# Performance work log

Hardware: AMD Instinct MI355X
Metric: run time of the kernel (lower is better)

The kernel has to match this reference:

```python
import jax, jax.numpy as jnp
import numpy as np

N, D_FEAT, T, H = 4000, 6, 60, 64


def _gru_layer(inp, Wih, Whh, bih, bhh):
    # inp: [N, T, in]; torch GRU gate math, gate order (r, z, n)
    x_proj = inp @ Wih.T + bih  # [N, T, 3H]
    h0 = jnp.zeros((inp.shape[0], Whh.shape[1]), inp.dtype)

    def step(h, xp):
        gh = h @ Whh.T + bhh
        xr, xz, xn = jnp.split(xp, 3, axis=-1)
        hr, hz, hn = jnp.split(gh, 3, axis=-1)
        r = jax.nn.sigmoid(xr + hr)
        z = jax.nn.sigmoid(xz + hz)
        n = jnp.tanh(xn + r * hn)
        h = (1.0 - z) * n + z * h
        return h, h

    _, hs = jax.lax.scan(step, h0, jnp.transpose(x_proj, (1, 0, 2)))  # [T, N, H]
    return jnp.transpose(hs, (1, 0, 2))  # [N, T, H]


def setup_inputs():
    key = jax.random.key(0)
    ks = jax.random.split(key, 16)
    s = 1.0 / np.sqrt(H)
    u = lambda k, shape: jax.random.uniform(k, shape, jnp.float32, -s, s)
    inp = {
        "x": jax.random.normal(ks[0], (N, D_FEAT * T), jnp.float32),
        "relation_matrix": jax.random.randint(ks[1], (N, N, 3), 0, 2).astype(jnp.float32),
        "W_ih0": u(ks[2], (3 * H, D_FEAT)),
        "W_hh0": u(ks[3], (3 * H, H)),
        "b_ih0": u(ks[4], (3 * H,)),
        "b_hh0": u(ks[5], (3 * H,)),
        "W_ih1": u(ks[6], (3 * H, H)),
        "W_hh1": u(ks[7], (3 * H, H)),
        "b_ih1": u(ks[8], (3 * H,)),
        "b_hh1": u(ks[9], (3 * H,)),
        "W": jax.random.normal(ks[10], (2 * H, 1), jnp.float32) * np.sqrt(6.0 / (2 * H + 1)),
        "b": jnp.zeros((), jnp.float32),
        "fc_w": u(ks[11], (1, 2 * H)),
        "fc_b": u(ks[12], (1,)),
    }
    return inp


def reference(x, relation_matrix, W_ih0, W_hh0, b_ih0, b_hh0,
              W_ih1, W_hh1, b_ih1, b_hh1, W, b, fc_w, fc_b):
    n = x.shape[0]
    # [N, d_feat*T] -> [N, T, d_feat]
    xh = jnp.transpose(x.reshape(n, D_FEAT, -1), (0, 2, 1))
    xh = _gru_layer(xh, W_ih0, W_hh0, b_ih0, b_hh0)
    xh = _gru_layer(xh, W_ih1, W_hh1, b_ih1, b_hh1)
    x_hidden = xh[:, -1, :]  # [N, H]

    # concat(ei, hidden_batch) @ W == a_i + c_j  (avoid O(N^2 * 2H) tensor)
    a = x_hidden @ W[:H, 0]   # [N]
    c = x_hidden @ W[H:, 0]   # [N]
    weight = jax.nn.leaky_relu(a[:, None] + c[None, :] + b, 0.01)  # [N, N]

    mask = relation_matrix.sum(axis=2)  # [N, N]
    valid_weight = jnp.where(mask == 0, -1000000.0, mask * weight)
    valid_weight = jax.nn.softmax(valid_weight, axis=1)

    hidden = valid_weight @ x_hidden            # [N, H]
    hidden = jnp.concatenate([x_hidden, hidden], axis=1)  # [N, 2H]
    pred = (hidden @ fc_w.T + fc_b).squeeze()   # [N]
    return pred
```

## Files before the change

kernel.cpp:

```cpp
#include <hip/hip_runtime.h>

#define NR 4000
#define TS 60
#define DF 6
#define HD 64
#define MB 16
#define ARB 32

typedef __attribute__((ext_vector_type(8))) short bf8_t;
typedef __attribute__((ext_vector_type(4))) short bf4_t;
typedef __attribute__((ext_vector_type(4))) float f32x4;

__device__ __forceinline__ float sigf(float x) { return 1.0f / (1.0f + __expf(-x)); }
__device__ __forceinline__ float tanhfast(float x) { return 1.0f - 2.0f / (1.0f + __expf(2.0f * x)); }

__device__ __forceinline__ unsigned short f2bf(float v) {
  union { float f; unsigned u; } x; x.f = v;
  unsigned r = (x.u + 0x7fffu + ((x.u >> 16) & 1u)) >> 16;
  return (unsigned short)r;
}
__device__ __forceinline__ float bf2f(unsigned short h) {
  union { unsigned u; float f; } y; y.u = ((unsigned)h) << 16; return y.f;
}
__device__ __forceinline__ void split8(const float* v, bf8_t& hi, bf8_t& lo) {
#pragma unroll
  for (int j = 0; j < 8; ++j) {
    unsigned short h = f2bf(v[j]);
    float rem = v[j] - bf2f(h);
    hi[j] = (short)h;
    lo[j] = (short)f2bf(rem);
  }
}

__global__ __launch_bounds__(256, 1) void gru_mfma(
    const float* __restrict__ x,
    const float* __restrict__ Wih0, const float* __restrict__ Whh0,
    const float* __restrict__ bih0, const float* __restrict__ bhh0,
    const float* __restrict__ Wih1, const float* __restrict__ Whh1,
    const float* __restrict__ bih1, const float* __restrict__ bhh1,
    const float* __restrict__ Wac,
    float* __restrict__ xh_out, float* __restrict__ a_out, float* __restrict__ c_out) {
  __shared__ float xldsT[TS][MB][12];
  __shared__ __align__(16) unsigned short h0hiL[2][16][76];
  __shared__ __align__(16) unsigned short h0loL[2][16][76];
  __shared__ __align__(16) unsigned short h1hiL[2][16][76];
  __shared__ __align__(16) unsigned short h1loL[2][16][76];
  __shared__ float red[2][4][MB];

  const int tid = threadIdx.x;
  const int w = tid >> 6;
  const int lane = tid & 63;
  const int lg = lane >> 4;
  const int lm = lane & 15;
  const int unit = w * 16 + lm;
  const int r0 = blockIdx.x * MB;

  for (int idx = tid; idx < MB * 360; idx += 256) {
    int rr = idx / 360, cc = idx - rr * 360;
    int f = cc / 60, t = cc - f * 60;
    xldsT[t][rr][f] = x[(size_t)r0 * 360 + idx];
  }

  bf8_t wB[3][3][2][2];
  {
    const float* mats[3] = {Whh0, Wih1, Whh1};
#pragma unroll
    for (int m = 0; m < 3; ++m)
#pragma unroll
      for (int g = 0; g < 3; ++g)
#pragma unroll
        for (int kt = 0; kt < 2; ++kt) {
          const float* src = mats[m] + (size_t)(g * 64 + unit) * 64 + kt * 32 + 8 * lg;
          float v[8];
          *(float4*)&v[0] = *(const float4*)&src[0];
          *(float4*)&v[4] = *(const float4*)&src[4];
          split8(v, wB[m][g][kt][0], wB[m][g][kt][1]);
        }
  }
  float wih0g[3][DF];
#pragma unroll
  for (int g = 0; g < 3; ++g)
#pragma unroll
    for (int f = 0; f < DF; ++f)
      wih0g[g][f] = Wih0[(size_t)(g * 64 + unit) * DF + f];

  const float bi0r = bih0[unit], bi0z = bih0[64 + unit], bi0n = bih0[128 + unit];
  const float bh0r = bhh0[unit], bh0z = bhh0[64 + unit], bh0n = bhh0[128 + unit];
  const float c1R = bih1[unit] + bhh1[unit];
  const float c1Z = bih1[64 + unit] + bhh1[64 + unit];
  const float b1xn = bih1[128 + unit], b1hn = bhh1[128 + unit];

  bf8_t a0[2][2], a1[2][2];
  bf8_t zf = {};
#pragma unroll
  for (int kt = 0; kt < 2; ++kt)
#pragma unroll
    for (int h = 0; h < 2; ++h) { a0[kt][h] = zf; a1[kt][h] = zf; }
  float h0c[4] = {0.f, 0.f, 0.f, 0.f};
  float h1c[4] = {0.f, 0.f, 0.f, 0.f};

  __syncthreads();

#define MF(acc, A, B) acc = __builtin_amdgcn_mfma_f32_16x16x32_bf16(A, B, acc, 0, 0, 0)
#define MF3(acc, Af, Bf) do { \
    MF(acc, Af[0], Bf[0]); MF(acc, Af[0], Bf[1]); MF(acc, Af[1], Bf[0]); } while (0)

  for (int p = 0; p <= TS; ++p) {
    const bool doL0 = (p < TS);
    const bool doL1 = (p >= 1);
    const int par = p & 1;
    f32x4 aR, aZ, aN;
    float xn0[4];
    if (doL0) {
#pragma unroll
      for (int i = 0; i < 4; ++i) {
        const int row = 4 * lg + i;
        const float* xb = &xldsT[p][row][0];
        float4 x4 = *(const float4*)xb;
        float2 x2 = *(const float2*)(xb + 4);
        float sr = bi0r, sz = bi0z, sn = bi0n;
        sr = fmaf(wih0g[0][0], x4.x, sr); sz = fmaf(wih0g[1][0], x4.x, sz); sn = fmaf(wih0g[2][0], x4.x, sn);
        sr = fmaf(wih0g[0][1], x4.y, sr); sz = fmaf(wih0g[1][1], x4.y, sz); sn = fmaf(wih0g[2][1], x4.y, sn);
        sr = fmaf(wih0g[0][2], x4.z, sr); sz = fmaf(wih0g[1][2], x4.z, sz); sn = fmaf(wih0g[2][2], x4.z, sn);
        sr = fmaf(wih0g[0][3], x4.w, sr); sz = fmaf(wih0g[1][3], x4.w, sz); sn = fmaf(wih0g[2][3], x4.w, sn);
        sr = fmaf(wih0g[0][4], x2.x, sr); sz = fmaf(wih0g[1][4], x2.x, sz); sn = fmaf(wih0g[2][4], x2.x, sn);
        sr = fmaf(wih0g[0][5], x2.y, sr); sz = fmaf(wih0g[1][5], x2.y, sz); sn = fmaf(wih0g[2][5], x2.y, sn);
        aR[i] = sr + bh0r;
        aZ[i] = sz + bh0z;
        aN[i] = bh0n;
        xn0[i] = sn;
      }
#pragma unroll
      for (int kt = 0; kt < 2; ++kt) {
        MF3(aR, a0[kt], wB[0][0][kt]);
        MF3(aZ, a0[kt], wB[0][1][kt]);
        MF3(aN, a0[kt], wB[0][2][kt]);
      }
    }
    f32x4 R1, Z1, XN, HN;
    if (doL1) {
#pragma unroll
      for (int i = 0; i < 4; ++i) { R1[i] = c1R; Z1[i] = c1Z; XN[i] = b1xn; HN[i] = b1hn; }
#pragma unroll
      for (int kt = 0; kt < 2; ++kt) {
        MF3(R1, a0[kt], wB[1][0][kt]);
        MF3(Z1, a0[kt], wB[1][1][kt]);
        MF3(XN, a0[kt], wB[1][2][kt]);
        MF3(R1, a1[kt], wB[2][0][kt]);
        MF3(Z1, a1[kt], wB[2][1][kt]);
        MF3(HN, a1[kt], wB[2][2][kt]);
      }
    }
    if (doL0) {
#pragma unroll
      for (int i = 0; i < 4; ++i) {
        float r = sigf(aR[i]);
        float z = sigf(aZ[i]);
        float n = tanhfast(xn0[i] + r * aN[i]);
        h0c[i] = n + z * (h0c[i] - n);
        const int row = 4 * lg + i;
        unsigned u = __float_as_uint(h0c[i]);
        h0hiL[par][row][unit] = (unsigned short)(u >> 16);
        float lo = h0c[i] - __uint_as_float(u & 0xffff0000u);
        h0loL[par][row][unit] = (unsigned short)(__float_as_uint(lo) >> 16);
      }
    }
    if (doL1) {
#pragma unroll
      for (int i = 0; i < 4; ++i) {
        float r = sigf(R1[i]);
        float z = sigf(Z1[i]);
        float n = tanhfast(XN[i] + r * HN[i]);
        h1c[i] = n + z * (h1c[i] - n);
      }
      if (p < TS) {
#pragma unroll
        for (int i = 0; i < 4; ++i) {
          const int row = 4 * lg + i;
          unsigned u = __float_as_uint(h1c[i]);
          h1hiL[par][row][unit] = (unsigned short)(u >> 16);
          float lo = h1c[i] - __uint_as_float(u & 0xffff0000u);
          h1loL[par][row][unit] = (unsigned short)(__float_as_uint(lo) >> 16);
        }
      }
    }
    __syncthreads();
    if (p < TS) {
#pragma unroll
      for (int kt = 0; kt < 2; ++kt) {
        const int cb = kt * 32 + 8 * lg;
        bf4_t u0 = *(const bf4_t*)&h0hiL[par][lm][cb];
        bf4_t u1 = *(const bf4_t*)&h0hiL[par][lm][cb + 4];
        a0[kt][0] = __builtin_shufflevector(u0, u1, 0, 1, 2, 3, 4, 5, 6, 7);
        bf4_t l0 = *(const bf4_t*)&h0loL[par][lm][cb];
        bf4_t l1 = *(const bf4_t*)&h0loL[par][lm][cb + 4];
        a0[kt][1] = __builtin_shufflevector(l0, l1, 0, 1, 2, 3, 4, 5, 6, 7);
      }
      if (p >= 1) {
#pragma unroll
        for (int kt = 0; kt < 2; ++kt) {
          const int cb = kt * 32 + 8 * lg;
          bf4_t u0 = *(const bf4_t*)&h1hiL[par][lm][cb];
          bf4_t u1 = *(const bf4_t*)&h1hiL[par][lm][cb + 4];
          a1[kt][0] = __builtin_shufflevector(u0, u1, 0, 1, 2, 3, 4, 5, 6, 7);
          bf4_t l0 = *(const bf4_t*)&h1loL[par][lm][cb];
          bf4_t l1 = *(const bf4_t*)&h1loL[par][lm][cb + 4];
          a1[kt][1] = __builtin_shufflevector(l0, l1, 0, 1, 2, 3, 4, 5, 6, 7);
        }
      }
    }
  }
#undef MF3
#undef MF

#pragma unroll
  for (int i = 0; i < 4; ++i)
    xh_out[(size_t)(r0 + 4 * lg + i) * HD + unit] = h1c[i];

  const float WaU = Wac[unit], WcU = Wac[64 + unit];
#pragma unroll
  for (int i = 0; i < 4; ++i) {
    float av = h1c[i] * WaU, cv = h1c[i] * WcU;
#pragma unroll
    for (int off = 1; off < 16; off <<= 1) {
      av += __shfl_xor(av, off, 64);
      cv += __shfl_xor(cv, off, 64);
    }
    if (lm == 0) {
      red[0][w][4 * lg + i] = av;
      red[1][w][4 * lg + i] = cv;
    }
  }
  __syncthreads();
  if (tid < MB) {
    a_out[r0 + tid] = red[0][0][tid] + red[0][1][tid] + red[0][2][tid] + red[0][3][tid];
    c_out[r0 + tid] = red[1][0][tid] + red[1][1][tid] + red[1][2][tid] + red[1][3][tid];
  }
}

__global__ __launch_bounds__(256) void attn_part(
    const float* __restrict__ rel,
    const float* __restrict__ xh,
    const float* __restrict__ aArr, const float* __restrict__ cArr,
    const float* __restrict__ bSc,
    float* __restrict__ part, int jsl, int lsp) {
  __shared__ float xhl[64][68];
  __shared__ float pbuf[ARB][64];
  __shared__ float cls[1024];

  const int tid = threadIdx.x;
  const int rg = tid >> 5;
  const int tk = tid & 31;
  const int bx = blockIdx.x;
  const int ib = bx >> lsp;
  const int js = bx & ((1 << lsp) - 1);
  const int jbeg = js * jsl;
  const int jend = (jbeg + jsl < NR) ? (jbeg + jsl) : NR;
  const int nch = (jend - jbeg + 63) >> 6;
  const float bb = bSc[0];

  int irow[4];
  float aib[4];
#pragma unroll
  for (int rr = 0; rr < 4; ++rr) {
    irow[rr] = ib * ARB + rg + 8 * rr;
    aib[rr] = aArr[irow[rr]] + bb;
  }

  for (int t = tid; t < jsl; t += 256)
    cls[t] = (jbeg + t < NR) ? cArr[jbeg + t] : 0.f;

  float pr[4][6];
#pragma unroll
  for (int rr = 0; rr < 4; ++rr) {
    const float* rp = rel + (size_t)irow[rr] * (3 * NR) + (size_t)(jbeg + 2 * tk) * 3;
#pragma unroll
    for (int e = 0; e < 6; ++e) pr[rr][e] = rp[e];
  }

  float m[4], s[4], acc0[4], acc1[4];
#pragma unroll
  for (int rr = 0; rr < 4; ++rr) { m[rr] = -3.0e38f; s[rr] = 0.f; acc0[rr] = 0.f; acc1[rr] = 0.f; }

  for (int c = 0; c < nch; ++c) {
    const int j0 = jbeg + c * 64;
    __syncthreads();
    {
      const int jj = tid >> 2, seg = tid & 3;
      const int j = j0 + jj;
      if (j < NR) {
        const float4* src = (const float4*)(xh + (size_t)j * 64 + seg * 16);
#pragma unroll
        for (int q = 0; q < 4; ++q) *(float4*)&xhl[jj][seg * 16 + 4 * q] = src[q];
      } else {
        float4 z = {0.f, 0.f, 0.f, 0.f};
#pragma unroll
        for (int q = 0; q < 4; ++q) *(float4*)&xhl[jj][seg * 16 + 4 * q] = z;
      }
    }

    const int jb = j0 + 2 * tk;
    const bool ok = (jb < jend);
    const int ci = c * 64 + 2 * tk;
    const float cl0 = cls[ci], cl1 = cls[ci + 1];

#pragma unroll
    for (int rr = 0; rr < 4; ++rr) {
      float msum0 = pr[rr][0] + pr[rr][1] + pr[rr][2];
      float msum1 = pr[rr][3] + pr[rr][4] + pr[rr][5];
      float w0 = aib[rr] + cl0, w1 = aib[rr] + cl1;
      w0 = (w0 > 0.f) ? w0 : 0.01f * w0;
      w1 = (w1 > 0.f) ? w1 : 0.01f * w1;
      float v0 = (!ok) ? -3.0e37f : ((msum0 == 0.f) ? -1.0e6f : msum0 * w0);
      float v1 = (!ok) ? -3.0e37f : ((msum1 == 0.f) ? -1.0e6f : msum1 * w1);

      float lm2 = fmaxf(v0, v1);
#pragma unroll
      for (int off = 16; off; off >>= 1) lm2 = fmaxf(lm2, __shfl_xor(lm2, off, 32));
      const float mn = fmaxf(m[rr], lm2);
      const float f = __expf(m[rr] - mn);
      const float p0 = __expf(v0 - mn);
      const float p1 = __expf(v1 - mn);
      float ls = p0 + p1;
#pragma unroll
      for (int off = 16; off; off >>= 1) ls += __shfl_xor(ls, off, 32);
      s[rr] = s[rr] * f + ls;
      acc0[rr] *= f;
      acc1[rr] *= f;
      m[rr] = mn;
      pbuf[rg + 8 * rr][2 * tk] = p0;
      pbuf[rg + 8 * rr][2 * tk + 1] = p1;
    }

    if (c + 1 < nch) {
      const int jn = j0 + 64 + 2 * tk;
      if (jn < jend) {
#pragma unroll
        for (int rr = 0; rr < 4; ++rr) {
          const float* rp = rel + (size_t)irow[rr] * (3 * NR) + (size_t)jn * 3;
#pragma unroll
          for (int e = 0; e < 6; ++e) pr[rr][e] = rp[e];
        }
      }
    }

    __syncthreads();

#pragma unroll 2
    for (int j4 = 0; j4 < 16; ++j4) {
      float4 pv0 = *(const float4*)&pbuf[rg][4 * j4];
      float4 pv1 = *(const float4*)&pbuf[rg + 8][4 * j4];
      float4 pv2 = *(const float4*)&pbuf[rg + 16][4 * j4];
      float4 pv3 = *(const float4*)&pbuf[rg + 24][4 * j4];
      float2 x0 = *(const float2*)&xhl[4 * j4 + 0][2 * tk];
      float2 x1 = *(const float2*)&xhl[4 * j4 + 1][2 * tk];
      float2 x2 = *(const float2*)&xhl[4 * j4 + 2][2 * tk];
      float2 x3 = *(const float2*)&xhl[4 * j4 + 3][2 * tk];
      acc0[0] = fmaf(pv0.x, x0.x, acc0[0]); acc1[0] = fmaf(pv0.x, x0.y, acc1[0]);
      acc0[0] = fmaf(pv0.y, x1.x, acc0[0]); acc1[0] = fmaf(pv0.y, x1.y, acc1[0]);
      acc0[0] = fmaf(pv0.z, x2.x, acc0[0]); acc1[0] = fmaf(pv0.z, x2.y, acc1[0]);
      acc0[0] = fmaf(pv0.w, x3.x, acc0[0]); acc1[0] = fmaf(pv0.w, x3.y, acc1[0]);
      acc0[1] = fmaf(pv1.x, x0.x, acc0[1]); acc1[1] = fmaf(pv1.x, x0.y, acc1[1]);
      acc0[1] = fmaf(pv1.y, x1.x, acc0[1]); acc1[1] = fmaf(pv1.y, x1.y, acc1[1]);
      acc0[1] = fmaf(pv1.z, x2.x, acc0[1]); acc1[1] = fmaf(pv1.z, x2.y, acc1[1]);
      acc0[1] = fmaf(pv1.w, x3.x, acc0[1]); acc1[1] = fmaf(pv1.w, x3.y, acc1[1]);
      acc0[2] = fmaf(pv2.x, x0.x, acc0[2]); acc1[2] = fmaf(pv2.x, x0.y, acc1[2]);
      acc0[2] = fmaf(pv2.y, x1.x, acc0[2]); acc1[2] = fmaf(pv2.y, x1.y, acc1[2]);
      acc0[2] = fmaf(pv2.z, x2.x, acc0[2]); acc1[2] = fmaf(pv2.z, x2.y, acc1[2]);
      acc0[2] = fmaf(pv2.w, x3.x, acc0[2]); acc1[2] = fmaf(pv2.w, x3.y, acc1[2]);
      acc0[3] = fmaf(pv3.x, x0.x, acc0[3]); acc1[3] = fmaf(pv3.x, x0.y, acc1[3]);
      acc0[3] = fmaf(pv3.y, x1.x, acc0[3]); acc1[3] = fmaf(pv3.y, x1.y, acc1[3]);
      acc0[3] = fmaf(pv3.z, x2.x, acc0[3]); acc1[3] = fmaf(pv3.z, x2.y, acc1[3]);
      acc0[3] = fmaf(pv3.w, x3.x, acc0[3]); acc1[3] = fmaf(pv3.w, x3.y, acc1[3]);
    }
  }

#pragma unroll
  for (int rr = 0; rr < 4; ++rr) {
    float* base = part + ((size_t)bx * ARB + rg + 8 * rr) * 66;
    if (tk == 0) { base[0] = m[rr]; base[1] = s[rr]; }
    base[2 + 2 * tk] = acc0[rr];
    base[3 + 2 * tk] = acc1[rr];
  }
}

__global__ __launch_bounds__(256) void attn_combine(
    const float* __restrict__ part,
    const float* __restrict__ xh,
    const float* __restrict__ fcw, const float* __restrict__ fcb,
    float* __restrict__ pred, int nsplit) {
  const int tid = threadIdx.x;
  const int r = blockIdx.x * 4 + (tid >> 6);
  const int lane = tid & 63;
  const int ib = r / ARB, il = r % ARB;

  float mstar = -3.0e38f;
  for (int k = 0; k < nsplit; ++k) {
    const float* b = part + ((size_t)(ib * nsplit + k) * ARB + il) * 66;
    mstar = fmaxf(mstar, b[0]);
  }
  float sstar = 0.f, onum = 0.f;
  for (int k = 0; k < nsplit; ++k) {
    const float* b = part + ((size_t)(ib * nsplit + k) * ARB + il) * 66;
    const float wk = __expf(b[0] - mstar);
    sstar = fmaf(wk, b[1], sstar);
    onum = fmaf(wk, b[2 + lane], onum);
  }
  const float o = onum / sstar;
  float p = fcw[lane] * xh[(size_t)r * HD + lane] + fcw[64 + lane] * o;
#pragma unroll
  for (int off = 32; off; off >>= 1) p += __shfl_xor(p, off, 64);
  if (lane == 0) pred[r] = p + fcb[0];
}

extern "C" void kernel_launch(void* const* d_in, const int* in_sizes, int n_in,
                              void* d_out, int out_size, void* d_ws, size_t ws_size,
                              hipStream_t stream) {
  const float* x    = (const float*)d_in[0];
  const float* rel  = (const float*)d_in[1];
  const float* Wih0 = (const float*)d_in[2];
  const float* Whh0 = (const float*)d_in[3];
  const float* bih0 = (const float*)d_in[4];
  const float* bhh0 = (const float*)d_in[5];
  const float* Wih1 = (const float*)d_in[6];
  const float* Whh1 = (const float*)d_in[7];
  const float* bih1 = (const float*)d_in[8];
  const float* bhh1 = (const float*)d_in[9];
  const float* Wac  = (const float*)d_in[10];
  const float* bSc  = (const float*)d_in[11];
  const float* fcw  = (const float*)d_in[12];
  const float* fcb  = (const float*)d_in[13];

  float* xh   = (float*)d_ws;
  float* aA   = xh + (size_t)NR * HD;
  float* cA   = aA + NR;
  float* part = cA + NR;
  float* pred = (float*)d_out;

  const size_t headF = (size_t)NR * HD + 2 * NR;
  int nsplit = 16, lsp = 4;
  for (;;) {
    size_t needB = (headF + (size_t)(NR / ARB) * nsplit * ARB * 66) * 4;
    if (needB <= ws_size || nsplit == 4) break;
    nsplit >>= 1;
    lsp -= 1;
  }
  const int jsl = NR / nsplit;

  gru_mfma<<<NR / MB, 256, 0, stream>>>(x, Wih0, Whh0, bih0, bhh0, Wih1, Whh1,
                                        bih1, bhh1, Wac, xh, aA, cA);
  attn_part<<<(NR / ARB) * nsplit, 256, 0, stream>>>(rel, xh, aA, cA, bSc, part, jsl, lsp);
  attn_combine<<<NR / 4, 256, 0, stream>>>(part, xh, fcw, fcb, pred, nsplit);
}
```

Before: 184.6 us.

## Precompute uint8 relation mask sums in spare blocks alongside GRU kernel

Adds extra blocks to the GRU launch that stream the 192MB relation tensor and write a per-pair uint8 mask sum. This overlaps the dominant memory read with the latency-bound recurrent GRU work, which only uses a few blocks per CU. The attention kernel then reads 1 byte per pair instead of 12 bytes. The default split count also drops from 16 to 8, and an extra 16MB workspace write and read are added, with a fallback path when the workspace is too small.

```diff
diff --git a/kernel.cpp b/kernel.cpp
--- a/kernel.cpp
+++ b/kernel.cpp
@@ -6,6 +6,8 @@
 #define HD 64
 #define MB 16
 #define ARB 32
+#define GRUB (NR / MB)
+#define MSB 750
 
 typedef __attribute__((ext_vector_type(8))) short bf8_t;
 typedef __attribute__((ext_vector_type(4))) short bf4_t;
@@ -32,14 +34,16 @@
   }
 }
 
-__global__ __launch_bounds__(256, 1) void gru_mfma(
+__global__ __launch_bounds__(256, 1) void gru_and_msum(
     const float* __restrict__ x,
+    const float* __restrict__ rel,
     const float* __restrict__ Wih0, const float* __restrict__ Whh0,
     const float* __restrict__ bih0, const float* __restrict__ bhh0,
     const float* __restrict__ Wih1, const float* __restrict__ Whh1,
     const float* __restrict__ bih1, const float* __restrict__ bhh1,
     const float* __restrict__ Wac,
-    float* __restrict__ xh_out, float* __restrict__ a_out, float* __restrict__ c_out) {
+    float* __restrict__ xh_out, float* __restrict__ a_out, float* __restrict__ c_out,
+    unsigned char* __restrict__ msum8) {
   __shared__ float xldsT[TS][MB][12];
   __shared__ __align__(16) unsigned short h0hiL[2][16][76];
   __shared__ __align__(16) unsigned short h0loL[2][16][76];
@@ -48,12 +52,31 @@
   __shared__ float red[2][4][MB];
 
   const int tid = threadIdx.x;
+  const int bx = blockIdx.x;
+
+  if (bx >= GRUB) {
+    const int nmb = gridDim.x - GRUB;
+    const size_t ngroups = (size_t)NR * NR / 4;
+    const size_t stride = (size_t)nmb * 256;
+    for (size_t g = (size_t)(bx - GRUB) * 256 + tid; g < ngroups; g += stride) {
+      const float4* rp = (const float4*)(rel + 12 * g);
+      float4 v0 = rp[0], v1 = rp[1], v2 = rp[2];
+      uchar4 o;
+      o.x = (unsigned char)(v0.x + v0.y + v0.z);
+      o.y = (unsigned char)(v0.w + v1.x + v1.y);
+      o.z = (unsigned char)(v1.z + v1.w + v2.x);
+      o.w = (unsigned char)(v2.y + v2.z + v2.w);
+      *(uchar4*)&msum8[4 * g] = o;
+    }
+    return;
+  }
+
   const int w = tid >> 6;
   const int lane = tid & 63;
   const int lg = lane >> 4;
   const int lm = lane & 15;
   const int unit = w * 16 + lm;
-  const int r0 = blockIdx.x * MB;
+  const int r0 = bx * MB;
 
   for (int idx = tid; idx < MB * 360; idx += 256) {
     int rr = idx / 360, cc = idx - rr * 360;
@@ -238,15 +261,17 @@
   }
 }
 
+template <int UM>
 __global__ __launch_bounds__(256) void attn_part(
     const float* __restrict__ rel,
+    const unsigned char* __restrict__ msum8,
     const float* __restrict__ xh,
     const float* __restrict__ aArr, const float* __restrict__ cArr,
     const float* __restrict__ bSc,
     float* __restrict__ part, int jsl, int lsp) {
   __shared__ float xhl[64][68];
   __shared__ float pbuf[ARB][64];
-  __shared__ float cls[1024];
+  __shared__ float cls[2048];
 
   const int tid = threadIdx.x;
   const int rg = tid >> 5;
@@ -271,11 +296,16 @@
     cls[t] = (jbeg + t < NR) ? cArr[jbeg + t] : 0.f;
 
   float pr[4][6];
+  uchar2 pm[4];
 #pragma unroll
   for (int rr = 0; rr < 4; ++rr) {
-    const float* rp = rel + (size_t)irow[rr] * (3 * NR) + (size_t)(jbeg + 2 * tk) * 3;
-#pragma unroll
-    for (int e = 0; e < 6; ++e) pr[rr][e] = rp[e];
+    if (UM) {
+      pm[rr] = *(const uchar2*)&msum8[(size_t)irow[rr] * NR + jbeg + 2 * tk];
+    } else {
+      const float* rp = rel + (size_t)irow[rr] * (3 * NR) + (size_t)(jbeg + 2 * tk) * 3;
+#pragma unroll
+      for (int e = 0; e < 6; ++e) pr[rr][e] = rp[e];
+    }
   }
 
   float m[4], s[4], acc0[4], acc1[4];
@@ -306,8 +336,14 @@
 
 #pragma unroll
     for (int rr = 0; rr < 4; ++rr) {
-      float msum0 = pr[rr][0] + pr[rr][1] + pr[rr][2];
-      float msum1 = pr[rr][3] + pr[rr][4] + pr[rr][5];
+      float msum0, msum1;
+      if (UM) {
+        msum0 = (float)pm[rr].x;
+        msum1 = (float)pm[rr].y;
+      } else {
+        msum0 = pr[rr][0] + pr[rr][1] + pr[rr][2];
+        msum1 = pr[rr][3] + pr[rr][4] + pr[rr][5];
+      }
       float w0 = aib[rr] + cl0, w1 = aib[rr] + cl1;
       w0 = (w0 > 0.f) ? w0 : 0.01f * w0;
       w1 = (w1 > 0.f) ? w1 : 0.01f * w1;
@@ -337,9 +373,13 @@
       if (jn < jend) {
 #pragma unroll
         for (int rr = 0; rr < 4; ++rr) {
-          const float* rp = rel + (size_t)irow[rr] * (3 * NR) + (size_t)jn * 3;
-#pragma unroll
-          for (int e = 0; e < 6; ++e) pr[rr][e] = rp[e];
+          if (UM) {
+            pm[rr] = *(const uchar2*)&msum8[(size_t)irow[rr] * NR + jn];
+          } else {
+            const float* rp = rel + (size_t)irow[rr] * (3 * NR) + (size_t)jn * 3;
+#pragma unroll
+            for (int e = 0; e < 6; ++e) pr[rr][e] = rp[e];
+          }
         }
       }
     }
@@ -431,24 +471,42 @@
   const float* fcw  = (const float*)d_in[12];
   const float* fcb  = (const float*)d_in[13];
 
-  float* xh   = (float*)d_ws;
-  float* aA   = xh + (size_t)NR * HD;
-  float* cA   = aA + NR;
+  float* xh = (float*)d_ws;
+  float* aA = xh + (size_t)NR * HD;
+  float* cA = aA + NR;
   float* part = cA + NR;
   float* pred = (float*)d_out;
 
   const size_t headF = (size_t)NR * HD + 2 * NR;
-  int nsplit = 16, lsp = 4;
-  for (;;) {
-    size_t needB = (headF + (size_t)(NR / ARB) * nsplit * ARB * 66) * 4;
-    if (needB <= ws_size || nsplit == 4) break;
-    nsplit >>= 1;
-    lsp -= 1;
+  const size_t msumB = (size_t)NR * NR;
+  auto needB = [&](int ns, bool um) {
+    return (headF + (size_t)(NR / ARB) * ns * ARB * 66) * 4 + (um ? msumB : 0);
+  };
+  bool use_msum = true;
+  int nsplit = 8, lsp = 3;
+  if (needB(8, true) > ws_size) {
+    if (needB(4, true) <= ws_size) { nsplit = 4; lsp = 2; }
+    else if (needB(2, true) <= ws_size) { nsplit = 2; lsp = 1; }
+    else {
+      use_msum = false;
+      if (needB(8, false) <= ws_size) { nsplit = 8; lsp = 3; }
+      else { nsplit = 4; lsp = 2; }
+    }
   }
   const int jsl = NR / nsplit;
-
-  gru_mfma<<<NR / MB, 256, 0, stream>>>(x, Wih0, Whh0, bih0, bhh0, Wih1, Whh1,
-                                        bih1, bhh1, Wac, xh, aA, cA);
-  attn_part<<<(NR / ARB) * nsplit, 256, 0, stream>>>(rel, xh, aA, cA, bSc, part, jsl, lsp);
+  unsigned char* msum8 =
+      (unsigned char*)(part + (size_t)(NR / ARB) * nsplit * ARB * 66);
+
+  const int nblk = use_msum ? (GRUB + MSB) : GRUB;
+  gru_and_msum<<<nblk, 256, 0, stream>>>(x, rel, Wih0, Whh0, bih0, bhh0,
+                                         Wih1, Whh1, bih1, bhh1, Wac,
+                                         xh, aA, cA, msum8);
+  if (use_msum) {
+    attn_part<1><<<(NR / ARB) * nsplit, 256, 0, stream>>>(
+        rel, msum8, xh, aA, cA, bSc, part, jsl, lsp);
+  } else {
+    attn_part<0><<<(NR / ARB) * nsplit, 256, 0, stream>>>(
+        rel, msum8, xh, aA, cA, bSc, part, jsl, lsp);
+  }
   attn_combine<<<NR / 4, 256, 0, stream>>>(part, xh, fcw, fcb, pred, nsplit);
 }
```

Result: slower. 207.8 us (+12.6%).

## Stage relation-matrix tiles through LDS with coalesced float4 loads, fix split at 8

Applied to the files above, without the earlier changes.

Adds a specialised attention-partial kernel that loads each 64-column chunk of the 32 relation rows into shared memory with wide float4 loads. Before this, each thread loaded six scalars per row into registers. The kernel is specialised to 8 column splits with constant trip counts, down from the previous default of 16. It targets the cost of streaming the large relation tensor with narrow per-thread loads. In exchange it drops the register prefetch of the next chunk and adds an extra barrier per chunk. Its larger shared-memory footprint may also lower occupancy. The old path is kept as a fallback when the workspace is small.

```diff
diff --git a/kernel.cpp b/kernel.cpp
--- a/kernel.cpp
+++ b/kernel.cpp
@@ -238,25 +238,26 @@
   }
 }
 
-__global__ __launch_bounds__(256) void attn_part(
+__global__ __launch_bounds__(256) void attn_part_lds(
     const float* __restrict__ rel,
     const float* __restrict__ xh,
     const float* __restrict__ aArr, const float* __restrict__ cArr,
     const float* __restrict__ bSc,
-    float* __restrict__ part, int jsl, int lsp) {
+    float* __restrict__ part) {
   __shared__ float xhl[64][68];
   __shared__ float pbuf[ARB][64];
-  __shared__ float cls[1024];
+  __shared__ float cls[512];
+  __shared__ float relL[32][200];
 
   const int tid = threadIdx.x;
   const int rg = tid >> 5;
   const int tk = tid & 31;
   const int bx = blockIdx.x;
-  const int ib = bx >> lsp;
-  const int js = bx & ((1 << lsp) - 1);
+  const int ib = bx >> 3;
+  const int js = bx & 7;
+  const int jsl = NR / 8;
   const int jbeg = js * jsl;
-  const int jend = (jbeg + jsl < NR) ? (jbeg + jsl) : NR;
-  const int nch = (jend - jbeg + 63) >> 6;
+  const int jend = jbeg + jsl;
   const float bb = bSc[0];
 
   int irow[4];
@@ -267,22 +268,14 @@
     aib[rr] = aArr[irow[rr]] + bb;
   }
 
-  for (int t = tid; t < jsl; t += 256)
-    cls[t] = (jbeg + t < NR) ? cArr[jbeg + t] : 0.f;
-
-  float pr[4][6];
-#pragma unroll
-  for (int rr = 0; rr < 4; ++rr) {
-    const float* rp = rel + (size_t)irow[rr] * (3 * NR) + (size_t)(jbeg + 2 * tk) * 3;
-#pragma unroll
-    for (int e = 0; e < 6; ++e) pr[rr][e] = rp[e];
-  }
+  for (int t = tid; t < 512; t += 256)
+    cls[t] = (t < jsl) ? cArr[jbeg + t] : 0.f;
 
   float m[4], s[4], acc0[4], acc1[4];
 #pragma unroll
   for (int rr = 0; rr < 4; ++rr) { m[rr] = -3.0e38f; s[rr] = 0.f; acc0[rr] = 0.f; acc1[rr] = 0.f; }
 
-  for (int c = 0; c < nch; ++c) {
+  for (int c = 0; c < 8; ++c) {
     const int j0 = jbeg + c * 64;
     __syncthreads();
     {
@@ -298,6 +291,17 @@
         for (int q = 0; q < 4; ++q) *(float4*)&xhl[jj][seg * 16 + 4 * q] = z;
       }
     }
+#pragma unroll
+    for (int k = 0; k < 6; ++k) {
+      const int fidx = k * 256 + tid;
+      const int sg = fidx / 48;
+      const int q = fidx - sg * 48;
+      int fo = j0 * 3 + 4 * q;
+      if (fo > 12000 - 4) fo = 0;
+      const float4 v = *(const float4*)(rel + (size_t)(ib * 32 + sg) * 12000 + fo);
+      *(float4*)&relL[sg][4 * q] = v;
+    }
+    __syncthreads();
 
     const int jb = j0 + 2 * tk;
     const bool ok = (jb < jend);
@@ -306,8 +310,12 @@
 
 #pragma unroll
     for (int rr = 0; rr < 4; ++rr) {
-      float msum0 = pr[rr][0] + pr[rr][1] + pr[rr][2];
-      float msum1 = pr[rr][3] + pr[rr][4] + pr[rr][5];
+      const int qp = rg + 8 * rr;
+      float2 f0 = *(const float2*)&relL[qp][6 * tk];
+      float2 f1 = *(const float2*)&relL[qp][6 * tk + 2];
+      float2 f2 = *(const float2*)&relL[qp][6 * tk + 4];
+      float msum0 = f0.x + f0.y + f1.x;
+      float msum1 = f1.y + f2.x + f2.y;
       float w0 = aib[rr] + cl0, w1 = aib[rr] + cl1;
       w0 = (w0 > 0.f) ? w0 : 0.01f * w0;
       w1 = (w1 > 0.f) ? w1 : 0.01f * w1;
@@ -331,20 +339,6 @@
       pbuf[rg + 8 * rr][2 * tk] = p0;
       pbuf[rg + 8 * rr][2 * tk + 1] = p1;
     }
-
-    if (c + 1 < nch) {
-      const int jn = j0 + 64 + 2 * tk;
-      if (jn < jend) {
-#pragma unroll
-        for (int rr = 0; rr < 4; ++rr) {
-          const float* rp = rel + (size_t)irow[rr] * (3 * NR) + (size_t)jn * 3;
-#pragma unroll
-          for (int e = 0; e < 6; ++e) pr[rr][e] = rp[e];
-        }
-      }
-    }
-
-    __syncthreads();
 
 #pragma unroll 2
     for (int j4 = 0; j4 < 16; ++j4) {
@@ -384,6 +378,152 @@
   }
 }
 
+__global__ __launch_bounds__(256) void attn_part_direct(
+    const float* __restrict__ rel,
+    const float* __restrict__ xh,
+    const float* __restrict__ aArr, const float* __restrict__ cArr,
+    const float* __restrict__ bSc,
+    float* __restrict__ part, int jsl, int lsp) {
+  __shared__ float xhl[64][68];
+  __shared__ float pbuf[ARB][64];
+  __shared__ float cls[2048];
+
+  const int tid = threadIdx.x;
+  const int rg = tid >> 5;
+  const int tk = tid & 31;
+  const int bx = blockIdx.x;
+  const int ib = bx >> lsp;
+  const int js = bx & ((1 << lsp) - 1);
+  const int jbeg = js * jsl;
+  const int jend = (jbeg + jsl < NR) ? (jbeg + jsl) : NR;
+  const int nch = (jend - jbeg + 63) >> 6;
+  const float bb = bSc[0];
+
+  int irow[4];
+  float aib[4];
+#pragma unroll
+  for (int rr = 0; rr < 4; ++rr) {
+    irow[rr] = ib * ARB + rg + 8 * rr;
+    aib[rr] = aArr[irow[rr]] + bb;
+  }
+
+  for (int t = tid; t < jsl; t += 256)
+    cls[t] = (jbeg + t < NR) ? cArr[jbeg + t] : 0.f;
+
+  float pr[4][6];
+#pragma unroll
+  for (int rr = 0; rr < 4; ++rr) {
+    const float* rp = rel + (size_t)irow[rr] * (3 * NR) + (size_t)(jbeg + 2 * tk) * 3;
+#pragma unroll
+    for (int e = 0; e < 6; ++e) pr[rr][e] = rp[e];
+  }
+
+  float m[4], s[4], acc0[4], acc1[4];
+#pragma unroll
+  for (int rr = 0; rr < 4; ++rr) { m[rr] = -3.0e38f; s[rr] = 0.f; acc0[rr] = 0.f; acc1[rr] = 0.f; }
+
+  for (int c = 0; c < nch; ++c) {
+    const int j0 = jbeg + c * 64;
+    __syncthreads();
+    {
+      const int jj = tid >> 2, seg = tid & 3;
+      const int j = j0 + jj;
+      if (j < NR) {
+        const float4* src = (const float4*)(xh + (size_t)j * 64 + seg * 16);
+#pragma unroll
+        for (int q = 0; q < 4; ++q) *(float4*)&xhl[jj][seg * 16 + 4 * q] = src[q];
+      } else {
+        float4 z = {0.f, 0.f, 0.f, 0.f};
+#pragma unroll
+        for (int q = 0; q < 4; ++q) *(float4*)&xhl[jj][seg * 16 + 4 * q] = z;
+      }
+    }
+
+    const int jb = j0 + 2 * tk;
+    const bool ok = (jb < jend);
+    const int ci = c * 64 + 2 * tk;
+    const float cl0 = cls[ci], cl1 = cls[ci + 1];
+
+#pragma unroll
+    for (int rr = 0; rr < 4; ++rr) {
+      float msum0 = pr[rr][0] + pr[rr][1] + pr[rr][2];
+      float msum1 = pr[rr][3] + pr[rr][4] + pr[rr][5];
+      float w0 = aib[rr] + cl0, w1 = aib[rr] + cl1;
+      w0 = (w0 > 0.f) ? w0 : 0.01f * w0;
+      w1 = (w1 > 0.f) ? w1 : 0.01f * w1;
+      float v0 = (!ok) ? -3.0e37f : ((msum0 == 0.f) ? -1.0e6f : msum0 * w0);
+      float v1 = (!ok) ? -3.0e37f : ((msum1 == 0.f) ? -1.0e6f : msum1 * w1);
+
+      float lm2 = fmaxf(v0, v1);
+#pragma unroll
+      for (int off = 16; off; off >>= 1) lm2 = fmaxf(lm2, __shfl_xor(lm2, off, 32));
+      const float mn = fmaxf(m[rr], lm2);
+      const float f = __expf(m[rr] - mn);
+      const float p0 = __expf(v0 - mn);
+      const float p1 = __expf(v1 - mn);
+      float ls = p0 + p1;
+#pragma unroll
+      for (int off = 16; off; off >>= 1) ls += __shfl_xor(ls, off, 32);
+      s[rr] = s[rr] * f + ls;
+      acc0[rr] *= f;
+      acc1[rr] *= f;
+      m[rr] = mn;
+      pbuf[rg + 8 * rr][2 * tk] = p0;
+      pbuf[rg + 8 * rr][2 * tk + 1] = p1;
+    }
+
+    if (c + 1 < nch) {
+      const int jn = j0 + 64 + 2 * tk;
+      if (jn < jend) {
+#pragma unroll
+        for (int rr = 0; rr < 4; ++rr) {
+          const float* rp = rel + (size_t)irow[rr] * (3 * NR) + (size_t)jn * 3;
+#pragma unroll
+          for (int e = 0; e < 6; ++e) pr[rr][e] = rp[e];
+        }
+      }
+    }
+
+    __syncthreads();
+
+#pragma unroll 2
+    for (int j4 = 0; j4 < 16; ++j4) {
+      float4 pv0 = *(const float4*)&pbuf[rg][4 * j4];
+      float4 pv1 = *(const float4*)&pbuf[rg + 8][4 * j4];
+      float4 pv2 = *(const float4*)&pbuf[rg + 16][4 * j4];
+      float4 pv3 = *(const float4*)&pbuf[rg + 24][4 * j4];
+      float2 x0 = *(const float2*)&xhl[4 * j4 + 0][2 * tk];
+      float2 x1 = *(const float2*)&xhl[4 * j4 + 1][2 * tk];
+      float2 x2 = *(const float2*)&xhl[4 * j4 + 2][2 * tk];
+      float2 x3 = *(const float2*)&xhl[4 * j4 + 3][2 * tk];
+      acc0[0] = fmaf(pv0.x, x0.x, acc0[0]); acc1[0] = fmaf(pv0.x, x0.y, acc1[0]);
+      acc0[0] = fmaf(pv0.y, x1.x, acc0[0]); acc1[0] = fmaf(pv0.y, x1.y, acc1[0]);
+      acc0[0] = fmaf(pv0.z, x2.x, acc0[0]); acc1[0] = fmaf(pv0.z, x2.y, acc1[0]);
+      acc0[0] = fmaf(pv0.w, x3.x, acc0[0]); acc1[0] = fmaf(pv0.w, x3.y, acc1[0]);
+      acc0[1] = fmaf(pv1.x, x0.x, acc0[1]); acc1[1] = fmaf(pv1.x, x0.y, acc1[1]);
+      acc0[1] = fmaf(pv1.y, x1.x, acc0[1]); acc1[1] = fmaf(pv1.y, x1.y, acc1[1]);
+      acc0[1] = fmaf(pv1.z, x2.x, acc0[1]); acc1[1] = fmaf(pv1.z, x2.y, acc1[1]);
+      acc0[1] = fmaf(pv1.w, x3.x, acc0[1]); acc1[1] = fmaf(pv1.w, x3.y, acc1[1]);
+      acc0[2] = fmaf(pv2.x, x0.x, acc0[2]); acc1[2] = fmaf(pv2.x, x0.y, acc1[2]);
+      acc0[2] = fmaf(pv2.y, x1.x, acc0[2]); acc1[2] = fmaf(pv2.y, x1.y, acc1[2]);
+      acc0[2] = fmaf(pv2.z, x2.x, acc0[2]); acc1[2] = fmaf(pv2.z, x2.y, acc1[2]);
+      acc0[2] = fmaf(pv2.w, x3.x, acc0[2]); acc1[2] = fmaf(pv2.w, x3.y, acc1[2]);
+      acc0[3] = fmaf(pv3.x, x0.x, acc0[3]); acc1[3] = fmaf(pv3.x, x0.y, acc1[3]);
+      acc0[3] = fmaf(pv3.y, x1.x, acc0[3]); acc1[3] = fmaf(pv3.y, x1.y, acc1[3]);
+      acc0[3] = fmaf(pv3.z, x2.x, acc0[3]); acc1[3] = fmaf(pv3.z, x2.y, acc1[3]);
+      acc0[3] = fmaf(pv3.w, x3.x, acc0[3]); acc1[3] = fmaf(pv3.w, x3.y, acc1[3]);
+    }
+  }
+
+#pragma unroll
+  for (int rr = 0; rr < 4; ++rr) {
+    float* base = part + ((size_t)bx * ARB + rg + 8 * rr) * 66;
+    if (tk == 0) { base[0] = m[rr]; base[1] = s[rr]; }
+    base[2 + 2 * tk] = acc0[rr];
+    base[3 + 2 * tk] = acc1[rr];
+  }
+}
+
 __global__ __launch_bounds__(256) void attn_combine(
     const float* __restrict__ part,
     const float* __restrict__ xh,
@@ -431,24 +571,27 @@
   const float* fcw  = (const float*)d_in[12];
   const float* fcb  = (const float*)d_in[13];
 
-  float* xh   = (float*)d_ws;
-  float* aA   = xh + (size_t)NR * HD;
-  float* cA   = aA + NR;
+  float* xh = (float*)d_ws;
+  float* aA = xh + (size_t)NR * HD;
+  float* cA = aA + NR;
   float* part = cA + NR;
   float* pred = (float*)d_out;
 
   const size_t headF = (size_t)NR * HD + 2 * NR;
-  int nsplit = 16, lsp = 4;
-  for (;;) {
-    size_t needB = (headF + (size_t)(NR / ARB) * nsplit * ARB * 66) * 4;
-    if (needB <= ws_size || nsplit == 4) break;
-    nsplit >>= 1;
-    lsp -= 1;
-  }
+  auto needB = [&](int ns) {
+    return (headF + (size_t)(NR / ARB) * ns * ARB * 66) * 4;
+  };
+  int nsplit = 8, lsp = 3;
+  if (needB(8) > ws_size) { nsplit = 4; lsp = 2; }
   const int jsl = NR / nsplit;
 
   gru_mfma<<<NR / MB, 256, 0, stream>>>(x, Wih0, Whh0, bih0, bhh0, Wih1, Whh1,
                                         bih1, bhh1, Wac, xh, aA, cA);
-  attn_part<<<(NR / ARB) * nsplit, 256, 0, stream>>>(rel, xh, aA, cA, bSc, part, jsl, lsp);
+  if (nsplit == 8) {
+    attn_part_lds<<<(NR / ARB) * 8, 256, 0, stream>>>(rel, xh, aA, cA, bSc, part);
+  } else {
+    attn_part_direct<<<(NR / ARB) * nsplit, 256, 0, stream>>>(
+        rel, xh, aA, cA, bSc, part, jsl, lsp);
+  }
   attn_combine<<<NR / 4, 256, 0, stream>>>(part, xh, fcw, fcb, pred, nsplit);
 }
```

Measured after the change: 197.7 us. 7.1% more time.
